# Kernel tuning notes

Measured on AMD Instinct MI355X. Metric: run time of the kernel, lower is better.

Reference implementation:

```python
import jax, jax.numpy as jnp
import numpy as np


def lstm_dir(x, w_ih, w_hh, b, reverse):
    # x: [N, L, E]; torch gate order i, f, g, o; b = b_ih + b_hh combined
    if reverse:
        x = x[:, ::-1, :]
    H = w_hh.shape[1]
    N = x.shape[0]
    xg = jnp.einsum('nle,ge->nlg', x, w_ih) + b  # [N, L, 4H]
    def step(carry, xt):
        h, c = carry
        g = xt + h @ w_hh.T
        i, f, gg, o = jnp.split(g, 4, axis=-1)
        c = jax.nn.sigmoid(f) * c + jax.nn.sigmoid(i) * jnp.tanh(gg)
        h = jax.nn.sigmoid(o) * jnp.tanh(c)
        return (h, c), h
    init = (jnp.zeros((N, H), x.dtype), jnp.zeros((N, H), x.dtype))
    _, hs = jax.lax.scan(step, init, jnp.swapaxes(xg, 0, 1))
    hs = jnp.swapaxes(hs, 0, 1)  # [N, L, H]
    if reverse:
        hs = hs[:, ::-1, :]
    return hs


def setup_inputs() -> dict:
    key = jax.random.key(0)
    ks = jax.random.split(key, 10)
    B, D, S, V, E, H = 32, 32, 64, 32000, 256, 512
    tok = jax.random.randint(ks[0], (B, D, S), 1, V)
    slen = jax.random.randint(ks[1], (B, D), 8, S + 1)  # ragged sentence lengths
    docs = jnp.where(jnp.arange(S)[None, None, :] < slen[..., None], tok, 0)
    doc_lens = jax.random.randint(ks[2], (B,), 1, D + 1)  # ragged doc lengths
    embed_weight = jax.random.normal(ks[3], (V, E), jnp.float32) * 0.02
    def p(k, shp):
        return jax.random.normal(k, shp, jnp.float32) * 0.05
    return dict(
        docs=docs, doc_lens=doc_lens, max_doc_len=D,
        embed_weight=embed_weight,
        w_ih_f=p(ks[4], (4 * H, E)), w_hh_f=p(ks[5], (4 * H, H)), b_f=p(ks[6], (4 * H,)),
        w_ih_b=p(ks[7], (4 * H, E)), w_hh_b=p(ks[8], (4 * H, H)), b_b=p(ks[9], (4 * H,)),
    )


def reference(docs, doc_lens, max_doc_len, embed_weight, w_ih_f, w_hh_f, b_f, w_ih_b, w_hh_b, b_b):
    B, D, S = docs.shape
    sents = docs.reshape(B * D, S)                     # all sentences, incl. invalid slots
    sent_lens = jnp.sum(jnp.sign(sents), axis=1)       # nonzero-token count per sentence
    x = embed_weight[sents]                            # [BD, S, E]
    out_f = lstm_dir(x, w_ih_f, w_hh_f, b_f, False)
    out_b = lstm_dir(x, w_ih_b, w_hh_b, b_b, True)
    out = jnp.concatenate([out_f, out_b], axis=-1)     # [BD, S, 2H]
    # avg_pool1d over first sent_lens timesteps (segment mean)
    tmask = (jnp.arange(S)[None, :] < sent_lens[:, None]).astype(out.dtype)
    denom = jnp.maximum(sent_lens, 1).astype(out.dtype)
    pooled = jnp.sum(out * tmask[:, :, None], axis=1) / denom[:, None]  # [BD, 2H]
    pooled = pooled.reshape(B, D, -1)
    # pad_doc: zero out sentence slots beyond each doc_len (scatter-pad)
    dmask = jnp.arange(D)[None, :] < doc_lens[:, None]
    return jnp.where(dmask[:, :, None], pooled, jnp.zeros((), pooled.dtype))
```

## Files before the change

kernel.cpp:

```cpp
#include <hip/hip_runtime.h>
#include <hip/hip_bf16.h>
#include <hip/hip_cooperative_groups.h>

namespace cg = cooperative_groups;

typedef __attribute__((ext_vector_type(4))) float f32x4;
typedef __attribute__((ext_vector_type(8))) short s16x8;

#define SEQ   64
#define EMB   256
#define HID   512
#define NROW  1024
#define NTHR  512
#define NGRID 256
#define LDS_BYTES 98304
#define BSTRIDE 32

#define XB_OFF   0ull
#define WHH_OFF  (XB_OFF + 65536ull * EMB * 2)
#define WIH_OFF  (WHH_OFF + 2ull * 2048 * HID * 2)
#define HB_OFF   (WIH_OFF + 2ull * 2048 * EMB * 2)
#define SL_OFF   (HB_OFF + 4ull * NROW * HID * 2)
#define BAR_OFF  (SL_OFF + 4096ull)
#define XCDW_OFF (BAR_OFF + 8ull * BSTRIDE * 4ull)

__device__ __forceinline__ unsigned short f2bf(float f) {
    union { float f; unsigned u; } x; x.f = f;
    unsigned r = x.u + 0x7fffu + ((x.u >> 16) & 1u);
    return (unsigned short)(r >> 16);
}
__device__ __forceinline__ void cvt8(unsigned short* dst, const float* src) {
    f32x4 v0 = *(const f32x4*)src;
    f32x4 v1 = *(const f32x4*)(src + 4);
    s16x8 o;
    o[0] = (short)f2bf(v0[0]); o[1] = (short)f2bf(v0[1]);
    o[2] = (short)f2bf(v0[2]); o[3] = (short)f2bf(v0[3]);
    o[4] = (short)f2bf(v1[0]); o[5] = (short)f2bf(v1[1]);
    o[6] = (short)f2bf(v1[2]); o[7] = (short)f2bf(v1[3]);
    *(s16x8*)dst = o;
}
__device__ __forceinline__ float sigf(float x)  { return 1.0f / (1.0f + __expf(-x)); }
__device__ __forceinline__ float tanh_(float x) { return 2.0f / (1.0f + __expf(-2.0f * x)) - 1.0f; }

__global__ void __launch_bounds__(NTHR, 2)
lstm_enc(const int* __restrict__ docs, const int* __restrict__ doc_lens,
         const float* __restrict__ embed,
         const float* __restrict__ w_ih_f, const float* __restrict__ w_hh_f, const float* __restrict__ b_f,
         const float* __restrict__ w_ih_b, const float* __restrict__ w_hh_b, const float* __restrict__ b_b,
         float* __restrict__ out, unsigned char* __restrict__ ws)
{
    extern __shared__ unsigned short Wf[];

    unsigned short* xb  = (unsigned short*)(ws + XB_OFF);
    unsigned short* whh = (unsigned short*)(ws + WHH_OFF);
    unsigned short* wih = (unsigned short*)(ws + WIH_OFF);
    unsigned short* hb  = (unsigned short*)(ws + HB_OFF);
    int*       sl   = (int*)(ws + SL_OFF);
    unsigned*  bar  = (unsigned*)(ws + BAR_OFF);
    unsigned*  xcdw = (unsigned*)(ws + XCDW_OFF);

    const int tid = threadIdx.x;
    const int bid = blockIdx.x;
    const int gid = bid * NTHR + tid;

    for (int i = 0; i < 16; ++i) {
        int slot = gid + i * (NGRID * NTHR);
        int row = slot >> 5;
        int e   = (slot & 31) << 3;
        int tok = docs[row];
        cvt8(xb + (size_t)slot * 8, embed + (size_t)tok * EMB + e);
    }
    cvt8(whh + (size_t)gid * 8,             w_hh_f + (size_t)gid * 8);
    cvt8(whh + (size_t)(gid + 131072) * 8,  w_hh_b + (size_t)gid * 8);
    {
        int dir0 = gid >> 16;
        int idx  = gid & 65535;
        cvt8(wih + (size_t)gid * 8, (dir0 ? w_ih_b : w_ih_f) + (size_t)idx * 8);
    }
    {
        s16x8 z = {0,0,0,0,0,0,0,0};
        *(s16x8*)(hb + (size_t)gid * 8) = z;
    }
    if (gid < NROW) {
        int c = 0;
        const int* dr = docs + gid * SEQ;
        for (int s2 = 0; s2 < SEQ; ++s2) c += (dr[s2] != 0);
        sl[gid] = c;
    }
    if (gid < 8 * BSTRIDE) bar[gid] = 0u;

    if (tid == 0) {
        unsigned xcd_id;
        asm("s_getreg_b32 %0, hwreg(HW_REG_XCC_ID)" : "=s"(xcd_id));
        __hip_atomic_store(xcdw + bid, xcd_id, __ATOMIC_RELAXED, __HIP_MEMORY_SCOPE_AGENT);
    }

    cg::this_grid().sync();

    const int grp = bid & 7;
    const int dir = grp >> 2;
    const int rg  = grp & 3;
    const int cgd = bid >> 3;
    const int rowbase = rg * 256;
    const int hubase  = cgd * 16;
    unsigned* mybar = bar + grp * BSTRIDE;

    bool fast;
    {
        unsigned mine = __hip_atomic_load(xcdw + bid, __ATOMIC_RELAXED, __HIP_MEMORY_SCOPE_AGENT);
        unsigned same = 1u;
        for (int j = 0; j < 32; ++j) {
            unsigned o = __hip_atomic_load(xcdw + (grp + 8 * j), __ATOMIC_RELAXED, __HIP_MEMORY_SCOPE_AGENT);
            same &= (o == mine) ? 1u : 0u;
        }
        fast = (same != 0u);
    }

    {
        const unsigned short* whh_d = whh + (size_t)dir * 2048 * HID;
        const unsigned short* wih_d = wih + (size_t)dir * 2048 * EMB;
        for (int s2 = 0; s2 < 12; ++s2) {
            int S = s2 * NTHR + tid;
            int f = S >> 6, lane_s = S & 63;
            int kc = f >> 2, g = f & 3;
            int l15s = lane_s & 15, lqs = lane_s >> 4;
            int gn = g * HID + hubase + l15s;
            int k  = kc * 32 + lqs * 8;
            const unsigned short* src = (k < HID)
                ? (whh_d + (size_t)gn * HID + k)
                : (wih_d + (size_t)gn * EMB + (k - HID));
            *(s16x8*)(Wf + (size_t)S * 8) = *(const s16x8*)src;
        }
    }
    __syncthreads();

    const int wid = tid >> 6, lane = tid & 63, l15 = lane & 15, lq = lane >> 4;
    const int hu = hubase + l15;
    const float* bsrc = dir ? b_b : b_f;
    float bg4[4];
    #pragma unroll
    for (int g = 0; g < 4; ++g) bg4[g] = bsrc[g * HID + hu];

    int rA[2];
    rA[0] = rowbase + wid * 32 + l15;
    rA[1] = rowbase + wid * 32 + 16 + l15;

    int gr8[8]; int sl8[8]; float c8[8], pool8[8];
    #pragma unroll
    for (int rf = 0; rf < 2; ++rf)
        #pragma unroll
        for (int r = 0; r < 4; ++r) {
            int k8 = rf * 4 + r;
            gr8[k8] = rowbase + wid * 32 + rf * 16 + lq * 4 + r;
            sl8[k8] = sl[gr8[k8]];
            c8[k8] = 0.f; pool8[k8] = 0.f;
        }

    f32x4 acc[2][4];

    auto ldB = [&](s16x8* dst, int kc) {
        #pragma unroll
        for (int g = 0; g < 4; ++g)
            dst[g] = *(const s16x8*)(Wf + ((size_t)(kc * 4 + g) * 64 + lane) * 8);
    };
    auto ldX = [&](s16x8* dst, int kc, int te2) {
        #pragma unroll
        for (int rf = 0; rf < 2; ++rf)
            dst[rf] = *(const s16x8*)(xb + ((size_t)rA[rf] * SEQ + te2) * EMB + (kc - 16) * 32 + lq * 8);
    };
    auto ldH = [&](s16x8* dst, int kc, const unsigned short* hsrc) {
        #pragma unroll
        for (int rf = 0; rf < 2; ++rf)
            dst[rf] = *(const s16x8*)(hsrc + (size_t)rA[rf] * HID + kc * 32 + lq * 8);
    };
    auto xpart = [&](int te2) {
        #pragma unroll
        for (int rf = 0; rf < 2; ++rf)
            #pragma unroll
            for (int g = 0; g < 4; ++g)
                acc[rf][g] = (f32x4){bg4[g], bg4[g], bg4[g], bg4[g]};
        s16x8 Ax[3][2];
        ldX(Ax[0], 16, te2);
        ldX(Ax[1], 17, te2);
        #pragma unroll
        for (int i = 0; i < 8; ++i) {
            if (i + 2 < 8) ldX(Ax[(i + 2) % 3], 18 + i, te2);
            s16x8 Bf[4]; ldB(Bf, 16 + i);
            #pragma unroll
            for (int rf = 0; rf < 2; ++rf)
                #pragma unroll
                for (int g = 0; g < 4; ++g)
                    acc[rf][g] = __builtin_amdgcn_mfma_f32_16x16x32_bf16(
                        Ax[i % 3][rf], Bf[g], acc[rf][g], 0, 0, 0);
        }
    };

    xpart(dir ? (SEQ - 1) : 0);

    #pragma unroll 1
    for (int t = 0; t < SEQ; ++t) {
        const int te = dir ? (SEQ - 1 - t) : t;
        const unsigned short* hrd = hb + (size_t)((t & 1) * 2 + dir) * NROW * HID;
        unsigned short* hwr       = hb + (size_t)((((t + 1) & 1)) * 2 + dir) * NROW * HID;

        __syncthreads();
        if (tid == 0) {
            unsigned tgt = 32u * (unsigned)t;
            while (__hip_atomic_load(mybar, __ATOMIC_RELAXED, __HIP_MEMORY_SCOPE_AGENT) < tgt)
                __builtin_amdgcn_s_sleep(1);
            if (fast) {
                asm volatile("buffer_inv" ::: "memory");
            } else {
                (void)__hip_atomic_load(mybar, __ATOMIC_ACQUIRE, __HIP_MEMORY_SCOPE_AGENT);
            }
        }
        __syncthreads();

        {
            s16x8 Ah[3][2];
            ldH(Ah[0], 0, hrd);
            ldH(Ah[1], 1, hrd);
            #pragma unroll
            for (int i = 0; i < 16; ++i) {
                if (i + 2 < 16) ldH(Ah[(i + 2) % 3], i + 2, hrd);
                s16x8 Bf[4]; ldB(Bf, i);
                #pragma unroll
                for (int rf = 0; rf < 2; ++rf)
                    #pragma unroll
                    for (int g = 0; g < 4; ++g)
                        acc[rf][g] = __builtin_amdgcn_mfma_f32_16x16x32_bf16(
                            Ah[i % 3][rf], Bf[g], acc[rf][g], 0, 0, 0);
            }
        }

        unsigned short hv8[8];
        #pragma unroll
        for (int rf = 0; rf < 2; ++rf) {
            #pragma unroll
            for (int r = 0; r < 4; ++r) {
                int k8 = rf * 4 + r;
                float iv = acc[rf][0][r];
                float fv = acc[rf][1][r];
                float gv = acc[rf][2][r];
                float ov = acc[rf][3][r];
                float cc = sigf(fv) * c8[k8] + sigf(iv) * tanh_(gv);
                c8[k8] = cc;
                float hh = sigf(ov) * tanh_(cc);
                hv8[k8] = f2bf(hh);
                if (te < sl8[k8]) pool8[k8] += hh;
            }
        }
        if (fast) {
            #pragma unroll
            for (int k8 = 0; k8 < 8; ++k8)
                hwr[(size_t)gr8[k8] * HID + hu] = hv8[k8];
        } else {
            #pragma unroll
            for (int k8 = 0; k8 < 8; ++k8)
                __hip_atomic_store(hwr + (size_t)gr8[k8] * HID + hu, hv8[k8],
                                   __ATOMIC_RELAXED, __HIP_MEMORY_SCOPE_AGENT);
        }

        __syncthreads();
        if (t < SEQ - 1) {
            if (tid == 0)
                __hip_atomic_fetch_add(mybar, 1u, __ATOMIC_RELAXED, __HIP_MEMORY_SCOPE_AGENT);
            xpart(dir ? (SEQ - 2 - t) : (t + 1));
        }
    }

    #pragma unroll
    for (int k8 = 0; k8 < 8; ++k8) {
        int gr = gr8[k8];
        int b = gr >> 5, d = gr & 31;
        float denom = (float)(sl8[k8] > 0 ? sl8[k8] : 1);
        float v = (d < doc_lens[b]) ? (pool8[k8] / denom) : 0.f;
        out[(size_t)gr * 1024 + (size_t)dir * HID + hu] = v;
    }
}

extern "C" void kernel_launch(void* const* d_in, const int* in_sizes, int n_in,
                              void* d_out, int out_size, void* d_ws, size_t ws_size,
                              hipStream_t stream) {
    const int*   docs     = (const int*)d_in[0];
    const int*   doc_lens = (const int*)d_in[1];
    const float* embed    = (const float*)d_in[3];
    const float* w_ih_f   = (const float*)d_in[4];
    const float* w_hh_f   = (const float*)d_in[5];
    const float* b_f      = (const float*)d_in[6];
    const float* w_ih_b   = (const float*)d_in[7];
    const float* w_hh_b   = (const float*)d_in[8];
    const float* b_b      = (const float*)d_in[9];
    float* out = (float*)d_out;
    unsigned char* wsp = (unsigned char*)d_ws;

    (void)in_sizes; (void)n_in; (void)out_size; (void)ws_size;

    hipFuncSetAttribute((const void*)lstm_enc,
                        hipFuncAttributeMaxDynamicSharedMemorySize, LDS_BYTES);

    void* args[] = { &docs, &doc_lens, &embed, &w_ih_f, &w_hh_f, &b_f,
                     &w_ih_b, &w_hh_b, &b_b, &out, &wsp };
    hipLaunchCooperativeKernel((void*)lstm_enc, dim3(NGRID), dim3(NTHR),
                               args, (unsigned)LDS_BYTES, stream);
}
```

Measured before the change: 1.013 ms.

## Replace atomic counter barrier with per-block flags polled by one wavefront

New measurement: 965.9 us. -4.7%, faster.

```diff
diff --git a/kernel.cpp b/kernel.cpp
--- a/kernel.cpp
+++ b/kernel.cpp
@@ -42,6 +42,14 @@
 __device__ __forceinline__ float sigf(float x)  { return 1.0f / (1.0f + __expf(-x)); }
 __device__ __forceinline__ float tanh_(float x) { return 2.0f / (1.0f + __expf(-2.0f * x)) - 1.0f; }
 
+__device__ __forceinline__ unsigned ld_flag_sc0(const unsigned* p) {
+    unsigned v;
+    asm volatile("global_load_dword %0, %1, off sc0\n\t"
+                 "s_waitcnt vmcnt(0)"
+                 : "=v"(v) : "v"(p) : "memory");
+    return v;
+}
+
 __global__ void __launch_bounds__(NTHR, 2)
 lstm_enc(const int* __restrict__ docs, const int* __restrict__ doc_lens,
          const float* __restrict__ embed,
@@ -103,7 +111,8 @@
     const int cgd = bid >> 3;
     const int rowbase = rg * 256;
     const int hubase  = cgd * 16;
-    unsigned* mybar = bar + grp * BSTRIDE;
+    unsigned* gflags  = bar + grp * BSTRIDE;
+    unsigned* myflag  = gflags + cgd;
 
     bool fast;
     {
@@ -203,33 +212,36 @@
         const unsigned short* hrd = hb + (size_t)((t & 1) * 2 + dir) * NROW * HID;
         unsigned short* hwr       = hb + (size_t)((((t + 1) & 1)) * 2 + dir) * NROW * HID;
 
-        __syncthreads();
-        if (tid == 0) {
-            unsigned tgt = 32u * (unsigned)t;
-            while (__hip_atomic_load(mybar, __ATOMIC_RELAXED, __HIP_MEMORY_SCOPE_AGENT) < tgt)
-                __builtin_amdgcn_s_sleep(1);
+        if (tid < 64) {
+            const unsigned tgt = (unsigned)t;
+            const bool act = (lane < 32);
+            const unsigned* fp = gflags + (lane & 31);
             if (fast) {
+                while (__ballot(act && (ld_flag_sc0(fp) < tgt)) != 0ull) {}
                 asm volatile("buffer_inv" ::: "memory");
             } else {
-                (void)__hip_atomic_load(mybar, __ATOMIC_ACQUIRE, __HIP_MEMORY_SCOPE_AGENT);
+                while (__ballot(act && (__hip_atomic_load(fp, __ATOMIC_RELAXED,
+                                        __HIP_MEMORY_SCOPE_AGENT) < tgt)) != 0ull) {}
+                (void)__hip_atomic_load(gflags, __ATOMIC_ACQUIRE, __HIP_MEMORY_SCOPE_AGENT);
             }
         }
         __syncthreads();
 
         {
-            s16x8 Ah[3][2];
+            s16x8 Ah[4][2];
             ldH(Ah[0], 0, hrd);
             ldH(Ah[1], 1, hrd);
+            ldH(Ah[2], 2, hrd);
             #pragma unroll
             for (int i = 0; i < 16; ++i) {
-                if (i + 2 < 16) ldH(Ah[(i + 2) % 3], i + 2, hrd);
+                if (i + 3 < 16) ldH(Ah[(i + 3) & 3], i + 3, hrd);
                 s16x8 Bf[4]; ldB(Bf, i);
                 #pragma unroll
                 for (int rf = 0; rf < 2; ++rf)
                     #pragma unroll
                     for (int g = 0; g < 4; ++g)
                         acc[rf][g] = __builtin_amdgcn_mfma_f32_16x16x32_bf16(
-                            Ah[i % 3][rf], Bf[g], acc[rf][g], 0, 0, 0);
+                            Ah[i & 3][rf], Bf[g], acc[rf][g], 0, 0, 0);
             }
         }
 
@@ -263,8 +275,14 @@
 
         __syncthreads();
         if (t < SEQ - 1) {
-            if (tid == 0)
-                __hip_atomic_fetch_add(mybar, 1u, __ATOMIC_RELAXED, __HIP_MEMORY_SCOPE_AGENT);
+            if (tid == 0) {
+                if (fast)
+                    __hip_atomic_store(myflag, (unsigned)(t + 1),
+                                       __ATOMIC_RELAXED, __HIP_MEMORY_SCOPE_WORKGROUP);
+                else
+                    __hip_atomic_store(myflag, (unsigned)(t + 1),
+                                       __ATOMIC_RELAXED, __HIP_MEMORY_SCOPE_AGENT);
+            }
             xpart(dir ? (SEQ - 2 - t) : (t + 1));
         }
     }
```
